# Performance work log

Measured on AMD Instinct MI355X. Metric: run time of the kernel, lower is better.

## Reference

```python
import math
import jax, jax.numpy as jnp
import numpy as np

N, D, H, K = 200000, 512, 256, 64  # stocks, input_size, hidden_size, latent_size (heads)


def setup_inputs() -> dict:
    key = jax.random.key(0)
    ks = jax.random.split(key, 11)
    s = 0.02  # weight init scale
    return {
        "e": jax.random.normal(ks[0], (N, D), dtype=jnp.float32),
        "q": jax.random.normal(ks[1], (K, H), dtype=jnp.float32),  # learnable query per head
        "Wk": jax.random.normal(ks[2], (K, H, D), dtype=jnp.float32) * s,
        "bk": jax.random.normal(ks[3], (K, H), dtype=jnp.float32) * s,
        "Wv": jax.random.normal(ks[4], (K, H, D), dtype=jnp.float32) * s,
        "bv": jax.random.normal(ks[5], (K, H), dtype=jnp.float32) * s,
        "mu_w": jax.random.normal(ks[6], (H,), dtype=jnp.float32) * s,
        "mu_b": jax.random.normal(ks[7], (), dtype=jnp.float32) * s,
        "sigma_w": jax.random.normal(ks[8], (H,), dtype=jnp.float32) * s,
        "sigma_b": jax.random.normal(ks[9], (), dtype=jnp.float32) * s,
    }


def reference(e, q, Wk, bk, Wv, bv, mu_w, mu_b, sigma_w, sigma_b):
    # Per head k: scores = q . (Wk @ e_i + bk) / sqrt(H)   -> [K, N]
    # Computed as (q @ Wk) @ e.T + q.bk, avoiding the [K, N, H] key tensor.
    scale = 1.0 / math.sqrt(H)
    qWk = jnp.einsum('kh,khd->kd', q, Wk)                      # [K, D]
    scores = (jnp.einsum('kd,nd->kn', qWk, e)
              + jnp.einsum('kh,kh->k', q, bk)[:, None]) * scale  # [K, N]
    attn = jax.nn.softmax(scores, axis=-1)                     # softmax over stocks
    # h_att = attn @ (e @ Wv.T + bv); since attn sums to 1, bias term is bv exactly.
    pooled = jnp.einsum('kn,nd->kd', attn, e)                  # [K, D]
    h_multi = jnp.einsum('kd,khd->kh', pooled, Wv) + bv        # [K, H]
    mu_prior = h_multi @ mu_w + mu_b                           # [K]
    sigma_prior = jnp.exp(h_multi @ sigma_w + sigma_b)         # [K]
    return mu_prior, sigma_prior
```

## Files before the change

kernel.cpp:

```cpp
#include <hip/hip_runtime.h>
#include <math.h>
#include <stdint.h>

#define NROWS 200000
#define DDIM  512
#define HDIM  256
#define KHEADS 64
#define NB    32
#define NITER (NROWS / NB)
#define GRID  512

typedef __attribute__((ext_vector_type(8))) short bf16x8;
typedef __attribute__((ext_vector_type(4))) float f32x4;

__device__ __forceinline__ uint32_t f2bf1(float x) {
    uint32_t u = __float_as_uint(x);
    return (u + 0x7FFFu + ((u >> 16) & 1u)) >> 16;
}
__device__ __forceinline__ uint32_t pk2(float a, float b) {
    uint32_t r;
    asm("v_cvt_pk_bf16_f32 %0, %1, %2" : "=v"(r) : "v"(a), "v"(b));
    return r;
}

__global__ __launch_bounds__(256)
void prep(const float* __restrict__ q, const float* __restrict__ Wk,
          const float* __restrict__ bk,
          unsigned short* __restrict__ qwkb, float* __restrict__ qbk)
{
    if (blockIdx.x == 512) {
        const int k = threadIdx.x;
        if (k < KHEADS) {
            const float4* q4 = (const float4*)(q + (k << 8));
            const float4* b4 = (const float4*)(bk + (k << 8));
            float s = 0.f;
            #pragma unroll 8
            for (int i = 0; i < 64; ++i) {
                float4 a = q4[i], b = b4[i];
                s += a.x * b.x + a.y * b.y + a.z * b.z + a.w * b.w;
            }
            qbk[k] = s * 0.0625f;
        }
        return;
    }
    const int k    = blockIdx.x >> 3;
    const int dq   = blockIdx.x & 7;
    const int t    = threadIdx.x;
    const int cd   = t & 63;
    const int hseg = t >> 6;
    const int d    = dq * 64 + cd;
    const float* wk = Wk + ((size_t)k << 17);
    const float* qk = q + (k << 8);
    const float* wp = wk + (hseg * 64) * 512 + d;
    const float* qp = qk + hseg * 64;
    float s0 = 0.f, s1 = 0.f, s2 = 0.f, s3 = 0.f;
    #pragma unroll 4
    for (int h = 0; h < 64; h += 4) {
        s0 = fmaf(qp[h],     wp[(h    ) * 512], s0);
        s1 = fmaf(qp[h + 1], wp[(h + 1) * 512], s1);
        s2 = fmaf(qp[h + 2], wp[(h + 2) * 512], s2);
        s3 = fmaf(qp[h + 3], wp[(h + 3) * 512], s3);
    }
    float s = (s0 + s1) + (s2 + s3);
    __shared__ float red[4][64];
    red[hseg][cd] = s;
    __syncthreads();
    if (t < 64) {
        float tot = (red[0][t] + red[1][t]) + (red[2][t] + red[3][t]);
        qwkb[(k << 9) + dq * 64 + t] = (unsigned short)f2bf1(tot * 0.0625f);
    }
}

__global__ __launch_bounds__(256, 2)
void fused_attn(const float* __restrict__ e,
                const unsigned short* __restrict__ qwkb,
                const float* __restrict__ qbk,
                float* __restrict__ pooled, float* __restrict__ lsum,
                float* __restrict__ parts, float* __restrict__ lparts,
                int use_parts)
{
    __shared__ char lds[65536];

    const int t    = threadIdx.x;
    const int w    = t >> 6;
    const int lane = t & 63;
    const int c    = lane & 15;
    const int Q    = lane >> 4;

    bf16x8 bq[16];
    {
        const char* qb_ = (const char*)qwkb + (w * 16 + c) * 1024 + Q * 16;
        #pragma unroll
        for (int ks = 0; ks < 16; ++ks)
            bq[ks] = *(const bf16x8*)(qb_ + ks * 64);
    }
    const float qbias = qbk[w * 16 + c];

    f32x4 acc[32];
    #pragma unroll
    for (int i = 0; i < 32; ++i) { f32x4 z = {0.f, 0.f, 0.f, 0.f}; acc[i] = z; }
    float l_part = 0.f;

    for (int b = blockIdx.x; b < NITER; b += GRID) {
        __syncthreads();
        const float4* eg = (const float4*)(e + (size_t)b * (NB * DDIM));
        #pragma unroll
        for (int i = 0; i < 4; ++i) {
            const int bb = t + i * 256;
            const int rg = bb >> 7, dg = bb & 127;
            float4 v0 = eg[(rg * 4 + 0) * 128 + dg];
            float4 v1 = eg[(rg * 4 + 1) * 128 + dg];
            float4 v2 = eg[(rg * 4 + 2) * 128 + dg];
            float4 v3 = eg[(rg * 4 + 3) * 128 + dg];
            const float* r0 = (const float*)&v0;
            const float* r1 = (const float*)&v1;
            const float* r2 = (const float*)&v2;
            const float* r3 = (const float*)&v3;
            {
                const int chA  = (rg >> 2) * 16 + (dg >> 3);
                const int lnD  = ((dg >> 1) & 3) * 16;
                const int byA  = (dg & 1) * 8;
                const int base = chA * 1024 + byA;
                const int sw   = chA & 7;
                int ln0 = (((rg & 3) * 4 + 0) + lnD) ^ sw;
                int ln1 = (((rg & 3) * 4 + 1) + lnD) ^ sw;
                int ln2 = (((rg & 3) * 4 + 2) + lnD) ^ sw;
                int ln3 = (((rg & 3) * 4 + 3) + lnD) ^ sw;
                *(uint2*)(lds + base + ln0 * 16) = make_uint2(pk2(r0[0], r0[1]), pk2(r0[2], r0[3]));
                *(uint2*)(lds + base + ln1 * 16) = make_uint2(pk2(r1[0], r1[1]), pk2(r1[2], r1[3]));
                *(uint2*)(lds + base + ln2 * 16) = make_uint2(pk2(r2[0], r2[1]), pk2(r2[2], r2[3]));
                *(uint2*)(lds + base + ln3 * 16) = make_uint2(pk2(r3[0], r3[1]), pk2(r3[2], r3[3]));
            }
            {
                const int chB  = dg >> 2;
                const int lnR  = ((rg >> 1) & 3) * 16;
                const int byB  = (rg & 1) * 8;
                const int base = 32768 + chB * 1024 + byB;
                const int sw   = chB & 7;
                #pragma unroll
                for (int i3 = 0; i3 < 4; ++i3) {
                    int ln = (((dg & 3) * 4 + i3) + lnR) ^ sw;
                    *(uint2*)(lds + base + ln * 16) =
                        make_uint2(pk2(r0[i3], r1[i3]), pk2(r2[i3], r3[i3]));
                }
            }
        }
        __syncthreads();

        f32x4 c10 = {0.f, 0.f, 0.f, 0.f};
        f32x4 c11 = {0.f, 0.f, 0.f, 0.f};
        __builtin_amdgcn_s_setprio(1);
        #pragma unroll
        for (int ks = 0; ks < 16; ++ks) {
            const bf16x8 a0 = *(const bf16x8*)(lds + ks * 1024        + ((lane ^ (ks & 7)) * 16));
            const bf16x8 a1 = *(const bf16x8*)(lds + (16 + ks) * 1024 + ((lane ^ ((16 + ks) & 7)) * 16));
            c10 = __builtin_amdgcn_mfma_f32_16x16x32_bf16(a0, bq[ks], c10, 0, 0, 0);
            c11 = __builtin_amdgcn_mfma_f32_16x16x32_bf16(a1, bq[ks], c11, 0, 0, 0);
        }
        __builtin_amdgcn_s_setprio(0);

        float pe0[4], pe1[4];
        #pragma unroll
        for (int r = 0; r < 4; ++r) {
            pe0[r] = __expf(c10[r] + qbias);
            pe1[r] = __expf(c11[r] + qbias);
            l_part += pe0[r] + pe1[r];
        }

        float av[8];
        #pragma unroll
        for (int j = 0; j < 8; ++j) {
            int sq = (2 * Q + (j >> 2)) & 3;
            int sl = c + (sq << 4);
            float v0 = __shfl(pe0[j & 3], sl, 64);
            float v1 = __shfl(pe1[j & 3], sl, 64);
            av[j] = (Q >= 2) ? v1 : v0;
        }
        union { uint32_t u[4]; bf16x8 v; } a2;
        #pragma unroll
        for (int d2 = 0; d2 < 4; ++d2) a2.u[d2] = pk2(av[2 * d2], av[2 * d2 + 1]);

        __builtin_amdgcn_s_setprio(1);
        #pragma unroll
        for (int ntd = 0; ntd < 32; ++ntd) {
            const bf16x8 bf_ = *(const bf16x8*)(lds + 32768 + ntd * 1024 + ((lane ^ (ntd & 7)) * 16));
            acc[ntd] = __builtin_amdgcn_mfma_f32_16x16x32_bf16(a2.v, bf_, acc[ntd], 0, 0, 0);
        }
        __builtin_amdgcn_s_setprio(0);
    }

    float lt = l_part;
    lt += __shfl_xor(lt, 16, 64);
    lt += __shfl_xor(lt, 32, 64);

    if (use_parts) {
        float* pp = parts + (size_t)blockIdx.x * (KHEADS * DDIM);
        #pragma unroll
        for (int ntd = 0; ntd < 32; ++ntd)
            #pragma unroll
            for (int r = 0; r < 4; ++r)
                pp[(w * 16 + Q * 4 + r) * DDIM + ntd * 16 + c] = acc[ntd][r];
        if (Q == 0) lparts[blockIdx.x * KHEADS + w * 16 + c] = lt;
    } else {
        #pragma unroll
        for (int ntd = 0; ntd < 32; ++ntd)
            #pragma unroll
            for (int r = 0; r < 4; ++r)
                atomicAdd(&pooled[(w * 16 + Q * 4 + r) * DDIM + ntd * 16 + c], acc[ntd][r]);
        if (Q == 0) atomicAdd(&lsum[w * 16 + c], lt);
    }
}

__global__ __launch_bounds__(256)
void reduce_parts(const float* __restrict__ parts, const float* __restrict__ lparts,
                  float* __restrict__ pooled, float* __restrict__ lsum)
{
    const int t   = threadIdx.x;
    const int bid = blockIdx.x;
    if (bid < 512) {
        const int o4    = t & 15;
        const int chunk = t >> 4;
        const float4* p4 = (const float4*)parts;
        const int base4 = bid * 16 + o4;
        float4 s = make_float4(0.f, 0.f, 0.f, 0.f);
        #pragma unroll 8
        for (int b = chunk * 32; b < chunk * 32 + 32; ++b) {
            float4 v = p4[b * 8192 + base4];
            s.x += v.x; s.y += v.y; s.z += v.z; s.w += v.w;
        }
        __shared__ float4 red[16][16];
        red[chunk][o4] = s;
        __syncthreads();
        if (t < 16) {
            float4 a = red[0][t];
            #pragma unroll
            for (int i = 1; i < 16; ++i) {
                float4 v = red[i][t];
                a.x += v.x; a.y += v.y; a.z += v.z; a.w += v.w;
            }
            ((float4*)pooled)[bid * 16 + t] = a;
        }
    } else {
        const int k = t & 63, chunk = t >> 6;
        float s = 0.f;
        #pragma unroll 8
        for (int b = chunk * 128; b < chunk * 128 + 128; ++b)
            s += lparts[b * 64 + k];
        __shared__ float redl[4][64];
        redl[chunk][k] = s;
        __syncthreads();
        if (t < 64) lsum[t] = (redl[0][t] + redl[1][t]) + (redl[2][t] + redl[3][t]);
    }
}

__global__ __launch_bounds__(256)
void finalize_partial(const float* __restrict__ pooled, const float* __restrict__ lsum,
                      const float* __restrict__ Wv, const float* __restrict__ bv,
                      const float* __restrict__ mu_w, const float* __restrict__ sigma_w,
                      float* __restrict__ macc, float* __restrict__ sacc)
{
    const int k  = blockIdx.x >> 3;
    const int hg = blockIdx.x & 7;
    const int t  = threadIdx.x;
    __shared__ float pn[DDIM];
    __shared__ float sm[32], ss[32];
    const float inv_l = 1.0f / lsum[k];
    pn[t]       = pooled[(k << 9) + t] * inv_l;
    pn[t + 256] = pooled[(k << 9) + t + 256] * inv_l;
    __syncthreads();
    const int hi = t >> 3, ds = t & 7;
    const int h  = hg * 32 + hi;
    const float4* wv4 = (const float4*)(Wv + ((size_t)(k * 256 + h) << 9));
    const float4* pn4 = (const float4*)pn;
    float s = 0.f;
    #pragma unroll
    for (int i = 0; i < 16; ++i) {
        float4 a  = pn4[ds + i * 8];
        float4 b_ = wv4[ds + i * 8];
        s += a.x * b_.x + a.y * b_.y + a.z * b_.z + a.w * b_.w;
    }
    s += __shfl_down(s, 4, 64);
    s += __shfl_down(s, 2, 64);
    s += __shfl_down(s, 1, 64);
    if (ds == 0) {
        float hval = s + bv[(k << 8) + h];
        sm[hi] = hval * mu_w[h];
        ss[hi] = hval * sigma_w[h];
    }
    __syncthreads();
    if (t == 0) {
        float m = 0.f, sg = 0.f;
        for (int i = 0; i < 32; ++i) { m += sm[i]; sg += ss[i]; }
        atomicAdd(&macc[k], m);
        atomicAdd(&sacc[k], sg);
    }
}

__global__ void final_out(const float* __restrict__ macc, const float* __restrict__ sacc,
                          const float* __restrict__ mu_b, const float* __restrict__ sigma_b,
                          float* __restrict__ out)
{
    int k = threadIdx.x;
    out[k]          = macc[k] + mu_b[0];
    out[KHEADS + k] = __expf(sacc[k] + sigma_b[0]);
}

extern "C" void kernel_launch(void* const* d_in, const int* in_sizes, int n_in,
                              void* d_out, int out_size, void* d_ws, size_t ws_size,
                              hipStream_t stream)
{
    const float* e       = (const float*)d_in[0];
    const float* q       = (const float*)d_in[1];
    const float* Wk      = (const float*)d_in[2];
    const float* bk      = (const float*)d_in[3];
    const float* Wv      = (const float*)d_in[4];
    const float* bv      = (const float*)d_in[5];
    const float* mu_w    = (const float*)d_in[6];
    const float* mu_b    = (const float*)d_in[7];
    const float* sigma_w = (const float*)d_in[8];
    const float* sigma_b = (const float*)d_in[9];
    float* out = (float*)d_out;

    char* wsb = (char*)d_ws;
    unsigned short* qwkb = (unsigned short*)wsb;
    float* qbk    = (float*)(wsb + 65536);
    float* pooled = (float*)(wsb + 65792);
    float* lsum   = (float*)(wsb + 196864);
    float* macc   = (float*)(wsb + 197120);
    float* sacc   = (float*)(wsb + 197376);
    float* parts  = (float*)(wsb + 197632);
    float* lparts = (float*)(wsb + 197632 + (size_t)GRID * KHEADS * DDIM * 4);
    const size_t need = 197632 + (size_t)GRID * KHEADS * DDIM * 4 + (size_t)GRID * KHEADS * 4;
    const int use_parts = (ws_size >= need) ? 1 : 0;

    if (use_parts)
        (void)hipMemsetAsync(macc, 0, 512, stream);
    else
        (void)hipMemsetAsync(pooled, 0, 131072 + 768, stream);

    prep<<<513, 256, 0, stream>>>(q, Wk, bk, qwkb, qbk);
    fused_attn<<<GRID, 256, 0, stream>>>(e, qwkb, qbk, pooled, lsum, parts, lparts, use_parts);
    if (use_parts)
        reduce_parts<<<513, 256, 0, stream>>>(parts, lparts, pooled, lsum);
    finalize_partial<<<512, 256, 0, stream>>>(pooled, lsum, Wv, bv, mu_w, sigma_w, macc, sacc);
    final_out<<<1, 64, 0, stream>>>(macc, sacc, mu_b, sigma_b, out);
}
```

Measured before the change: 645.7 us.

## Fuse final output into finalize via ticket, vectorize prep, drop setprio

Removes the separate final_out launch: finalize_partial now takes a global ticket counter, and the last block to finish reads the accumulated sums and writes the outputs. The prep kernel is reworked so each thread loads float2 pairs over 8 h-segments and stores packed bf16 pairs, which should make the Wk loads wider. The s_setprio hints around the MFMA loops in fused_attn are removed. These are three unrelated changes, and the ticket scheme adds a threadfence and an extra atomic per block.

```diff
diff --git a/kernel.cpp b/kernel.cpp
--- a/kernel.cpp
+++ b/kernel.cpp
@@ -46,28 +46,29 @@
     const int k    = blockIdx.x >> 3;
     const int dq   = blockIdx.x & 7;
     const int t    = threadIdx.x;
-    const int cd   = t & 63;
-    const int hseg = t >> 6;
-    const int d    = dq * 64 + cd;
-    const float* wk = Wk + ((size_t)k << 17);
-    const float* qk = q + (k << 8);
-    const float* wp = wk + (hseg * 64) * 512 + d;
-    const float* qp = qk + hseg * 64;
-    float s0 = 0.f, s1 = 0.f, s2 = 0.f, s3 = 0.f;
+    const int cd   = t & 31;
+    const int hseg = t >> 5;
+    const int d0   = dq * 64 + cd * 2;
+    const float*  wk = Wk + ((size_t)k << 17);
+    const float*  qp = q + (k << 8) + hseg * 32;
+    const float2* wp = (const float2*)(wk + (size_t)(hseg * 32) * 512 + d0);
+    float2 s0 = make_float2(0.f, 0.f), s1 = make_float2(0.f, 0.f);
     #pragma unroll 4
-    for (int h = 0; h < 64; h += 4) {
-        s0 = fmaf(qp[h],     wp[(h    ) * 512], s0);
-        s1 = fmaf(qp[h + 1], wp[(h + 1) * 512], s1);
-        s2 = fmaf(qp[h + 2], wp[(h + 2) * 512], s2);
-        s3 = fmaf(qp[h + 3], wp[(h + 3) * 512], s3);
-    }
-    float s = (s0 + s1) + (s2 + s3);
-    __shared__ float red[4][64];
+    for (int h = 0; h < 32; h += 2) {
+        float2 a = wp[(h    ) * 256];
+        float2 b = wp[(h + 1) * 256];
+        s0.x = fmaf(qp[h],     a.x, s0.x); s0.y = fmaf(qp[h],     a.y, s0.y);
+        s1.x = fmaf(qp[h + 1], b.x, s1.x); s1.y = fmaf(qp[h + 1], b.y, s1.y);
+    }
+    float2 s = make_float2(s0.x + s1.x, s0.y + s1.y);
+    __shared__ float2 red[8][32];
     red[hseg][cd] = s;
     __syncthreads();
-    if (t < 64) {
-        float tot = (red[0][t] + red[1][t]) + (red[2][t] + red[3][t]);
-        qwkb[(k << 9) + dq * 64 + t] = (unsigned short)f2bf1(tot * 0.0625f);
+    if (t < 32) {
+        float2 tot = make_float2(0.f, 0.f);
+        #pragma unroll
+        for (int i = 0; i < 8; ++i) { tot.x += red[i][t].x; tot.y += red[i][t].y; }
+        ((uint32_t*)qwkb)[(k << 8) + dq * 32 + t] = pk2(tot.x * 0.0625f, tot.y * 0.0625f);
     }
 }
 
@@ -149,7 +150,6 @@
 
         f32x4 c10 = {0.f, 0.f, 0.f, 0.f};
         f32x4 c11 = {0.f, 0.f, 0.f, 0.f};
-        __builtin_amdgcn_s_setprio(1);
         #pragma unroll
         for (int ks = 0; ks < 16; ++ks) {
             const bf16x8 a0 = *(const bf16x8*)(lds + ks * 1024        + ((lane ^ (ks & 7)) * 16));
@@ -157,7 +157,6 @@
             c10 = __builtin_amdgcn_mfma_f32_16x16x32_bf16(a0, bq[ks], c10, 0, 0, 0);
             c11 = __builtin_amdgcn_mfma_f32_16x16x32_bf16(a1, bq[ks], c11, 0, 0, 0);
         }
-        __builtin_amdgcn_s_setprio(0);
 
         float pe0[4], pe1[4];
         #pragma unroll
@@ -180,13 +179,11 @@
         #pragma unroll
         for (int d2 = 0; d2 < 4; ++d2) a2.u[d2] = pk2(av[2 * d2], av[2 * d2 + 1]);
 
-        __builtin_amdgcn_s_setprio(1);
         #pragma unroll
         for (int ntd = 0; ntd < 32; ++ntd) {
             const bf16x8 bf_ = *(const bf16x8*)(lds + 32768 + ntd * 1024 + ((lane ^ (ntd & 7)) * 16));
             acc[ntd] = __builtin_amdgcn_mfma_f32_16x16x32_bf16(a2.v, bf_, acc[ntd], 0, 0, 0);
         }
-        __builtin_amdgcn_s_setprio(0);
     }
 
     float lt = l_part;
@@ -257,13 +254,16 @@
 void finalize_partial(const float* __restrict__ pooled, const float* __restrict__ lsum,
                       const float* __restrict__ Wv, const float* __restrict__ bv,
                       const float* __restrict__ mu_w, const float* __restrict__ sigma_w,
-                      float* __restrict__ macc, float* __restrict__ sacc)
+                      const float* __restrict__ mu_b, const float* __restrict__ sigma_b,
+                      float* __restrict__ macc, float* __restrict__ sacc,
+                      int* __restrict__ ticket, float* __restrict__ out)
 {
     const int k  = blockIdx.x >> 3;
     const int hg = blockIdx.x & 7;
     const int t  = threadIdx.x;
     __shared__ float pn[DDIM];
     __shared__ float sm[32], ss[32];
+    __shared__ int is_last;
     const float inv_l = 1.0f / lsum[k];
     pn[t]       = pooled[(k << 9) + t] * inv_l;
     pn[t + 256] = pooled[(k << 9) + t + 256] * inv_l;
@@ -293,16 +293,17 @@
         for (int i = 0; i < 32; ++i) { m += sm[i]; sg += ss[i]; }
         atomicAdd(&macc[k], m);
         atomicAdd(&sacc[k], sg);
-    }
-}
-
-__global__ void final_out(const float* __restrict__ macc, const float* __restrict__ sacc,
-                          const float* __restrict__ mu_b, const float* __restrict__ sigma_b,
-                          float* __restrict__ out)
-{
-    int k = threadIdx.x;
-    out[k]          = macc[k] + mu_b[0];
-    out[KHEADS + k] = __expf(sacc[k] + sigma_b[0]);
+        __threadfence();
+        int old = atomicAdd(ticket, 1);
+        is_last = (old == 511);
+    }
+    __syncthreads();
+    if (is_last && t < KHEADS) {
+        float m  = atomicAdd(&macc[t], 0.0f);
+        float sg = atomicAdd(&sacc[t], 0.0f);
+        out[t]          = m + mu_b[0];
+        out[KHEADS + t] = __expf(sg + sigma_b[0]);
+    }
 }
 
 extern "C" void kernel_launch(void* const* d_in, const int* in_sizes, int n_in,
@@ -328,20 +329,21 @@
     float* lsum   = (float*)(wsb + 196864);
     float* macc   = (float*)(wsb + 197120);
     float* sacc   = (float*)(wsb + 197376);
-    float* parts  = (float*)(wsb + 197632);
-    float* lparts = (float*)(wsb + 197632 + (size_t)GRID * KHEADS * DDIM * 4);
-    const size_t need = 197632 + (size_t)GRID * KHEADS * DDIM * 4 + (size_t)GRID * KHEADS * 4;
+    int*   ticket = (int*)  (wsb + 197632);
+    float* parts  = (float*)(wsb + 197888);
+    float* lparts = (float*)(wsb + 197888 + (size_t)GRID * KHEADS * DDIM * 4);
+    const size_t need = 197888 + (size_t)GRID * KHEADS * DDIM * 4 + (size_t)GRID * KHEADS * 4;
     const int use_parts = (ws_size >= need) ? 1 : 0;
 
     if (use_parts)
-        (void)hipMemsetAsync(macc, 0, 512, stream);
+        (void)hipMemsetAsync(macc, 0, 768, stream);
     else
-        (void)hipMemsetAsync(pooled, 0, 131072 + 768, stream);
+        (void)hipMemsetAsync(pooled, 0, 132096, stream);
 
     prep<<<513, 256, 0, stream>>>(q, Wk, bk, qwkb, qbk);
     fused_attn<<<GRID, 256, 0, stream>>>(e, qwkb, qbk, pooled, lsum, parts, lparts, use_parts);
     if (use_parts)
         reduce_parts<<<513, 256, 0, stream>>>(parts, lparts, pooled, lsum);
-    finalize_partial<<<512, 256, 0, stream>>>(pooled, lsum, Wv, bv, mu_w, sigma_w, macc, sacc);
-    final_out<<<1, 64, 0, stream>>>(macc, sacc, mu_b, sigma_b, out);
-}
+    finalize_partial<<<512, 256, 0, stream>>>(pooled, lsum, Wv, bv, mu_w, sigma_w,
+                                              mu_b, sigma_b, macc, sacc, ticket, out);
+}
```

Measured after the change: 647.1 us. About the same (+0.2%).
